# Kernel tuning notes

Hardware: AMD Instinct MI355X
Metric: run time of the kernel (lower is better)

Reference implementation:

```python
import jax, jax.numpy as jnp
import numpy as np

B, T, C = 2, 2048, 2048
N_HEAD = 16
HD = C // N_HEAD  # 128


def setup_inputs() -> dict:
    key = jax.random.key(0)
    k1, k2, k3, k4, k5 = jax.random.split(key, 5)
    s_in = 1.0 / np.sqrt(C)
    return {
        "x": jax.random.normal(k1, (B, T, C), dtype=jnp.float32),
        # weights stored as (in, out), i.e. transpose of torch Linear weight
        "W_attn": jax.random.normal(k2, (C, 3 * C), dtype=jnp.float32) * s_in,
        "b_attn": jax.random.normal(k3, (3 * C,), dtype=jnp.float32) * 0.02,
        "W_proj": jax.random.normal(k4, (C, C), dtype=jnp.float32) * s_in,
        "b_proj": jax.random.normal(k5, (C,), dtype=jnp.float32) * 0.02,
    }


def reference(x, W_attn, b_attn, W_proj, b_proj):
    # qkv projection: (B,T,3C)
    qkv = x @ W_attn + b_attn
    q, k, v = jnp.split(qkv, 3, axis=-1)
    # (B, n_head, T, head_dim)
    q = q.reshape(B, T, N_HEAD, HD).transpose(0, 2, 1, 3)
    k = k.reshape(B, T, N_HEAD, HD).transpose(0, 2, 1, 3)
    v = v.reshape(B, T, N_HEAD, HD).transpose(0, 2, 1, 3)
    # scores (B,H,T,T), causal mask (T_q == T_k prefill path)
    att = jnp.einsum("bhqd,bhkd->bhqk", q, k) * (1.0 / np.sqrt(HD))
    causal = jnp.tril(jnp.ones((T, T), dtype=bool))
    att = jnp.where(causal[None, None], att, -jnp.inf)
    att = jax.nn.softmax(att, axis=-1)  # attn_dropout is identity (p=0)
    y = jnp.einsum("bhqk,bhkd->bhqd", att, v)
    y = y.transpose(0, 2, 1, 3).reshape(B, T, C)
    y = y @ W_proj + b_proj  # resid_dropout identity (p=0)
    # new_cache = (k, v, T) since T == block_size; return output tensor
    return y
```

## Files before the change

kernel.cpp:

```cpp
#include <hip/hip_runtime.h>
#include <cstdint>
#include <cstddef>


typedef __bf16 bf16x8 __attribute__((ext_vector_type(8)));
typedef float  f32x4  __attribute__((ext_vector_type(4)));
typedef unsigned short u16x4 __attribute__((ext_vector_type(4)));
typedef unsigned short u16x8 __attribute__((ext_vector_type(8)));

__device__ __forceinline__ unsigned short f2bf(float f) {
  unsigned int u = __builtin_bit_cast(unsigned int, f);
  u += 0x7fffu + ((u >> 16) & 1u);
  return (unsigned short)(u >> 16);
}

__device__ __forceinline__ void gld16(void* lds, const void* g) {
  __builtin_amdgcn_global_load_lds(
      (const __attribute__((address_space(1))) void*)g,
      (__attribute__((address_space(3))) void*)lds, 16, 0, 0);
}

__device__ __forceinline__ unsigned lds_addr(const void* p) {
  return (unsigned)(size_t)(const __attribute__((address_space(3))) void*)p;
}

__device__ __forceinline__ bf16x8 ds_read16(unsigned addr) {
  bf16x8 r;
  asm volatile("ds_read_b128 %0, %1" : "=v"(r) : "v"(addr));
  return r;
}

__device__ __forceinline__ void ds_write8(unsigned addr, u16x4 d) {
  unsigned long long v = __builtin_bit_cast(unsigned long long, d);
  asm volatile("ds_write_b64 %0, %1" :: "v"(addr), "v"(v));
}

__global__ void cvt_f32_bf16_k(const float* __restrict__ in,
                               unsigned short* __restrict__ out, int n4) {
  int i = blockIdx.x * blockDim.x + threadIdx.x;
  int stride = gridDim.x * blockDim.x;
  for (; i < n4; i += stride) {
    float4 v = ((const float4*)in)[i];
    ushort4 o;
    o.x = f2bf(v.x); o.y = f2bf(v.y); o.z = f2bf(v.z); o.w = f2bf(v.w);
    ((ushort4*)out)[i] = o;
  }
}

__global__ __launch_bounds__(256) void transpose_f32_bf16(
    const float* __restrict__ in, unsigned short* __restrict__ out,
    int R, int C) {
  __shared__ float tile[64][65];
  int c0 = blockIdx.x * 64, r0 = blockIdx.y * 64;
  int t = threadIdx.x;
  int lr = t >> 4, lc = (t & 15) * 4;
#pragma unroll
  for (int i = 0; i < 4; i++) {
    int row = lr + i * 16;
    float4 v = *(const float4*)&in[(size_t)(r0 + row) * C + c0 + lc];
    tile[row][lc] = v.x; tile[row][lc + 1] = v.y;
    tile[row][lc + 2] = v.z; tile[row][lc + 3] = v.w;
  }
  __syncthreads();
  int wr = t >> 3, wc = (t & 7) * 8;
#pragma unroll
  for (int i = 0; i < 2; i++) {
    int crow = wr + i * 32;
    u16x8 o;
#pragma unroll
    for (int j = 0; j < 8; j++) o[j] = f2bf(tile[wc + j][crow]);
    *(u16x8*)&out[(size_t)(c0 + crow) * R + r0 + wc] = o;
  }
}

__global__ __launch_bounds__(256) void extract_vT_k(
    const unsigned short* __restrict__ qkv, unsigned short* __restrict__ vT) {
  __shared__ unsigned int tile32[64][33];
  int bh = blockIdx.z, b = bh >> 4, h = bh & 15;
  int t0 = blockIdx.x * 64, d0 = blockIdx.y * 64;
  int t = threadIdx.x;
  int lr = t >> 3, lc = (t & 7) * 8;
  const unsigned short* src = qkv + (size_t)(b * 2048) * 6144 + 4096 + h * 128;
#pragma unroll
  for (int i = 0; i < 2; i++) {
    int row = lr + i * 32;
    u16x8 v = *(const u16x8*)&src[(size_t)(t0 + row) * 6144 + d0 + lc];
#pragma unroll
    for (int j = 0; j < 8; j++) {
      unsigned short* p = (unsigned short*)&tile32[lc + j][row & 31];
      p[row >> 5] = v[j];
    }
  }
  __syncthreads();
  int dr = t >> 2, tc = (t & 3) * 8;
  u16x8 lo, hi;
#pragma unroll
  for (int j = 0; j < 8; j++) {
    unsigned int u = tile32[dr][tc + j];
    lo[j] = (unsigned short)(u & 0xffffu);
    hi[j] = (unsigned short)(u >> 16);
  }
  unsigned short* dst = vT + (size_t)bh * 128 * 2048 + (size_t)(d0 + dr) * 2048 + t0;
  *(u16x8*)&dst[tc] = lo;
  *(u16x8*)&dst[tc + 32] = hi;
}

template <int OUT_BF16>
__global__ __launch_bounds__(256) void gemm_bt(
    const unsigned short* __restrict__ A, const unsigned short* __restrict__ BT,
    const float* __restrict__ bias, void* __restrict__ Cout,
    int M, int N, int K) {
  __shared__ __align__(16) unsigned short sA[128 * 64];
  __shared__ __align__(16) unsigned short sB[128 * 64];

  const int tid = threadIdx.x, w = tid >> 6, lane = tid & 63;
  const int quad = lane >> 4, l16 = lane & 15;
  const int m0 = blockIdx.y * 128, n0 = blockIdx.x * 128;
  const int wr = w >> 1, wc = w & 1;

  const unsigned short* gA[4];
  const unsigned short* gB[4];
  unsigned short* lA[4];
  unsigned short* lB[4];
#pragma unroll
  for (int i = 0; i < 4; i++) {
    int c = w * 256 + i * 64 + lane;
    int row = c >> 3, scol = (c & 7) ^ (row & 7);
    gA[i] = A + (size_t)(m0 + row) * K + scol * 8;
    gB[i] = BT + (size_t)(n0 + row) * K + scol * 8;
    lA[i] = sA + (size_t)(w * 256 + i * 64) * 8;
    lB[i] = sB + (size_t)(w * 256 + i * 64) * 8;
  }

  f32x4 acc[4][4] = {};

  for (int k0 = 0; k0 < K; k0 += 64) {
#pragma unroll
    for (int i = 0; i < 4; i++) {
      gld16(lA[i], gA[i]); gld16(lB[i], gB[i]);
      gA[i] += 64; gB[i] += 64;
    }
    __syncthreads();

#pragma unroll
    for (int kk = 0; kk < 2; kk++) {
      const int cc = (kk * 4 + quad) ^ (l16 & 7);
      bf16x8 af[4], bfr[4];
#pragma unroll
      for (int mi = 0; mi < 4; mi++)
        af[mi] = *(const bf16x8*)&sA[(wr * 64 + mi * 16 + l16) * 64 + cc * 8];
#pragma unroll
      for (int ni = 0; ni < 4; ni++)
        bfr[ni] = *(const bf16x8*)&sB[(wc * 64 + ni * 16 + l16) * 64 + cc * 8];
#pragma unroll
      for (int mi = 0; mi < 4; mi++)
#pragma unroll
        for (int ni = 0; ni < 4; ni++)
          acc[mi][ni] = __builtin_amdgcn_mfma_f32_16x16x32_bf16(
              af[mi], bfr[ni], acc[mi][ni], 0, 0, 0);
    }
    __syncthreads();
  }

#pragma unroll
  for (int mi = 0; mi < 4; mi++) {
    int row = m0 + wr * 64 + mi * 16 + quad * 4;
#pragma unroll
    for (int ni = 0; ni < 4; ni++) {
      int col = n0 + wc * 64 + ni * 16 + l16;
      float bv = bias[col];
#pragma unroll
      for (int r = 0; r < 4; r++) {
        float v = acc[mi][ni][r] + bv;
        if (OUT_BF16)
          ((unsigned short*)Cout)[(size_t)(row + r) * N + col] = f2bf(v);
        else
          ((float*)Cout)[(size_t)(row + r) * N + col] = v;
      }
    }
  }
}

#define BARRIER8 __builtin_amdgcn_s_barrier()
#define WAIT_LGKM0 asm volatile("s_waitcnt lgkmcnt(0)" ::: "memory")
#define WAIT_LGKM4 asm volatile("s_waitcnt lgkmcnt(4)" ::: "memory")
#define SCHED0 __builtin_amdgcn_sched_barrier(0)
#define WAIT_VM4 asm volatile("s_waitcnt vmcnt(4)" ::: "memory")
#define WAIT_VM0 asm volatile("s_waitcnt vmcnt(0)" ::: "memory")

#define STAGE_A(buf, h, t)                                                   \
  do {                                                                       \
    gld16(&sA[buf][((h) * 1024 + w * 64) * 8],                               \
          gA0 + (size_t)(h) * 128 * K + (size_t)(t) * 64);                   \
    gld16(&sA[buf][((h) * 1024 + 512 + w * 64) * 8],                         \
          gA1 + (size_t)(h) * 128 * K + (size_t)(t) * 64);                   \
  } while (0)

#define STAGE_B(buf, h, t)                                                   \
  do {                                                                       \
    gld16(&sB[buf][((h) * 1024 + w * 64) * 8],                               \
          gB0 + (size_t)(h) * 128 * K + (size_t)(t) * 64);                   \
    gld16(&sB[buf][((h) * 1024 + 512 + w * 64) * 8],                         \
          gB1 + (size_t)(h) * 128 * K + (size_t)(t) * 64);                   \
  } while (0)

#define LDA4(buf, mh, kk)                                                    \
  do {                                                                       \
    const int cc_ = ((kk) * 4 + quad) ^ (l16 & 7);                           \
    _Pragma("unroll") for (int i_ = 0; i_ < 4; ++i_) {                       \
      const int rr_ = (mh) * 128 + wr * 64 + i_ * 16 + l16;                  \
      a_[i_] = ds_read16(lds_addr(&sA[buf][rr_ * 64 + cc_ * 8]));            \
    }                                                                        \
  } while (0)

#define LDB4(buf, kk)                                                        \
  do {                                                                       \
    const int cc_ = ((kk) * 4 + quad) ^ (l16 & 7);                           \
    _Pragma("unroll") for (int i_ = 0; i_ < 4; ++i_) {                       \
      const int rr_ = wc * 64 + i_ * 16 + l16;                               \
      b_[i_] = ds_read16(lds_addr(&sB[buf][rr_ * 64 + cc_ * 8]));            \
    }                                                                        \
  } while (0)

#define MM16(mh)                                                             \
  do {                                                                       \
    __builtin_amdgcn_s_setprio(1);                                           \
    _Pragma("unroll") for (int i_ = 0; i_ < 4; ++i_)                         \
    _Pragma("unroll") for (int n_ = 0; n_ < 4; ++n_)                         \
        acc[(mh) * 4 + i_][n_] = __builtin_amdgcn_mfma_f32_16x16x32_bf16(    \
            a_[i_], b_[n_], acc[(mh) * 4 + i_][n_], 0, 0, 0);                \
    __builtin_amdgcn_s_setprio(0);                                           \
  } while (0)

template <int OUT_BF16>
__global__ __launch_bounds__(512, 2) void gemm_bt8(
    const unsigned short* __restrict__ A, const unsigned short* __restrict__ BT,
    const float* __restrict__ bias, void* __restrict__ Cout,
    int M, int N, int K) {
  __shared__ __align__(16) unsigned short sA[2][256 * 64];
  __shared__ __align__(16) unsigned short sB[2][256 * 64];
  (void)M;

  const int tid = threadIdx.x, w = tid >> 6, lane = tid & 63;
  const int quad = lane >> 4, l16 = lane & 15;
  const int wr = w >> 2, wc = w & 3;

  const int nwgx = gridDim.x;
  const int nwg = nwgx * gridDim.y;
  const int wg = blockIdx.y * nwgx + blockIdx.x;
  const int q8 = nwg >> 3, r8 = nwg & 7;
  const int xcd = wg & 7, loc = wg >> 3;
  const int swz =
      (xcd < r8 ? xcd * (q8 + 1) : r8 * (q8 + 1) + (xcd - r8) * q8) + loc;
  const int m0 = (swz / nwgx) * 256;
  const int n0 = (swz % nwgx) * 256;

  const int c0 = tid, c1 = tid + 512;
  const int r0c = c0 >> 3, s0c = (c0 & 7) ^ (r0c & 7);
  const int r1c = c1 >> 3, s1c = (c1 & 7) ^ (r1c & 7);
  const unsigned short* gA0 = A + (size_t)(m0 + r0c) * K + s0c * 8;
  const unsigned short* gA1 = A + (size_t)(m0 + r1c) * K + s1c * 8;
  const unsigned short* gB0 = BT + (size_t)(n0 + r0c) * K + s0c * 8;
  const unsigned short* gB1 = BT + (size_t)(n0 + r1c) * K + s1c * 8;

  f32x4 acc[8][4] = {};
  bf16x8 a_[4], b_[4];

  const int NT = K >> 6;
  const int NI = NT >> 1;

  STAGE_B(0, 0, 0); STAGE_A(0, 0, 0);
  STAGE_B(0, 1, 0); STAGE_A(0, 1, 0);
  STAGE_B(1, 0, 1); STAGE_A(1, 0, 1);
  WAIT_VM4;
  BARRIER8;

  for (int i = 0; i < NI; ++i) {
    const int t1 = 2 * i + 1;
    const int tn0 = 2 * i + 2, tn1 = 2 * i + 3;
    const bool last = (i == NI - 1);

    LDB4(0, 0); LDA4(0, 0, 0);
    STAGE_B(1, 1, t1); STAGE_A(1, 1, t1);
    BARRIER8; WAIT_LGKM0; SCHED0; MM16(0); BARRIER8;

    LDA4(0, 1, 0);
    BARRIER8; WAIT_LGKM0; SCHED0; MM16(1); BARRIER8;

    LDB4(0, 1); LDA4(0, 0, 1);
    BARRIER8; WAIT_LGKM0; SCHED0; MM16(0); BARRIER8;

    LDA4(0, 1, 1);
    if (!last) {
      STAGE_B(0, 0, tn0); STAGE_A(0, 0, tn0);
      WAIT_VM4;
    } else {
      WAIT_VM0;
    }
    BARRIER8; WAIT_LGKM0; SCHED0; MM16(1); BARRIER8;

    LDB4(1, 0); LDA4(1, 0, 0);
    if (!last) { STAGE_B(0, 1, tn0); STAGE_A(0, 1, tn0); }
    BARRIER8; WAIT_LGKM0; SCHED0; MM16(0); BARRIER8;

    LDA4(1, 1, 0);
    BARRIER8; WAIT_LGKM0; SCHED0; MM16(1); BARRIER8;

    LDB4(1, 1); LDA4(1, 0, 1);
    BARRIER8; WAIT_LGKM0; SCHED0; MM16(0); BARRIER8;

    LDA4(1, 1, 1);
    if (!last) {
      STAGE_B(1, 0, tn1); STAGE_A(1, 0, tn1);
      WAIT_VM4;
    }
    BARRIER8; WAIT_LGKM0; SCHED0; MM16(1); BARRIER8;
  }

#pragma unroll
  for (int mi = 0; mi < 8; ++mi) {
    const int mh = mi >> 2, i2 = mi & 3;
    int row = m0 + mh * 128 + wr * 64 + i2 * 16 + quad * 4;
#pragma unroll
    for (int ni = 0; ni < 4; ++ni) {
      int col = n0 + wc * 64 + ni * 16 + l16;
      float bv = bias[col];
#pragma unroll
      for (int rr = 0; rr < 4; ++rr) {
        float v = acc[mi][ni][rr] + bv;
        if (OUT_BF16)
          ((unsigned short*)Cout)[(size_t)(row + rr) * N + col] = f2bf(v);
        else
          ((float*)Cout)[(size_t)(row + rr) * N + col] = v;
      }
    }
  }
}

#undef STAGE_A
#undef STAGE_B
#undef LDA4
#undef LDB4
#undef MM16

__global__ __launch_bounds__(256) void flash_attn(
    const unsigned short* __restrict__ qkv, const unsigned short* __restrict__ vT,
    unsigned short* __restrict__ yout) {
  __shared__ __align__(16) unsigned short sK[2][64 * 128];
  __shared__ __align__(16) unsigned short sVT[2][128 * 64];
  __shared__ __align__(16) unsigned short sP[4 * 16 * 64];

  const int tid = threadIdx.x, w = tid >> 6, lane = tid & 63;
  const int quad = lane >> 4, l16 = lane & 15;
  const int id = blockIdx.x;
  const int g = id & 31;
  const int qp = id >> 5;
  const int b = g >> 4, h = g & 15;
  const int T = 2048, CC = 6144, HD = 128;
  const float qscale = 0.12753257252f;

  const unsigned short* gK = qkv + (size_t)(b * T) * CC + 2048 + h * HD;
  const unsigned short* gV = vT + (size_t)(b * 16 + h) * HD * T;
  unsigned short* pw = sP + w * 16 * 64;

  const unsigned short* kSrc[4];
  const unsigned short* vSrc[4];
  unsigned short* kDst[4];
  unsigned short* vDst[4];
#pragma unroll
  for (int i = 0; i < 4; i++) {
    int c = w * 256 + i * 64 + lane;
    int kR = c >> 4, kC = (c & 15) ^ (kR & 15);
    int vR = c >> 3, vC = (c & 7) ^ (vR & 7);
    kSrc[i] = gK + (size_t)kR * CC + kC * 8;
    vSrc[i] = gV + (size_t)vR * T + vC * 8;
    kDst[i] = (unsigned short*)sK + (size_t)(w * 256 + i * 64) * 8;
    vDst[i] = (unsigned short*)sVT + (size_t)(w * 256 + i * 64) * 8;
  }
  const int KBUF = 64 * 128, VBUF = 128 * 64;

  const int qtA = qp, qtB = 31 - qp;
  int qt = qtA, kt = 0;

  bf16x8 qf[4];
  float m_old, l_sum;
  f32x4 o[8] = {};
  {
    const size_t qrow = (size_t)(b * T + qt * 64 + w * 16 + l16) * CC + h * HD;
#pragma unroll
    for (int kb = 0; kb < 4; kb++) {
      bf16x8 raw = *(const bf16x8*)&qkv[qrow + kb * 32 + quad * 8];
      bf16x8 sc;
#pragma unroll
      for (int j = 0; j < 8; j++) sc[j] = (__bf16)((float)raw[j] * qscale);
      qf[kb] = sc;
    }
  }
  m_old = -1e30f; l_sum = 0.f;

#pragma unroll
  for (int i = 0; i < 4; i++) {
    gld16(kDst[i], kSrc[i]);
    gld16(vDst[i], vSrc[i]);
  }

  const int total = qtA + qtB + 2;
  for (int it = 0; it < total; ++it) {
    __syncthreads();
    const int cur = it & 1;
    const bool segEnd = (kt == qt);

    if (it + 1 < total) {
      const int nkt = segEnd ? 0 : kt + 1;
      const int nb_ = (it + 1) & 1;
      const size_t kOff = (size_t)nkt * 64 * CC;
      const int vOff = nkt * 64;
#pragma unroll
      for (int i = 0; i < 4; i++) {
        gld16(kDst[i] + (size_t)nb_ * KBUF, kSrc[i] + kOff);
        gld16(vDst[i] + (size_t)nb_ * VBUF, vSrc[i] + vOff);
      }
    }

    const unsigned short* sKc = (const unsigned short*)sK + (size_t)cur * KBUF;
    const unsigned short* sVc = (const unsigned short*)sVT + (size_t)cur * VBUF;

    f32x4 s4[4] = {};
    bf16x8 kf[4], kg[4];
#pragma unroll
    for (int kb = 0; kb < 4; kb++) {
      int rr = kb * 16 + l16;
      int cc = quad ^ l16;
      kf[kb] = ds_read16(lds_addr(&sKc[rr * 128 + cc * 8]));
    }
#pragma unroll
    for (int dc = 0; dc < 4; dc++) {
      if (dc < 3) {
#pragma unroll
        for (int kb = 0; kb < 4; kb++) {
          int rr = kb * 16 + l16;
          int cc = ((dc + 1) * 4 + quad) ^ l16;
          kg[kb] = ds_read16(lds_addr(&sKc[rr * 128 + cc * 8]));
        }
        WAIT_LGKM4;
      } else {
        WAIT_LGKM0;
      }
      SCHED0;
      __builtin_amdgcn_s_setprio(1);
#pragma unroll
      for (int kb = 0; kb < 4; kb++)
        s4[kb] = __builtin_amdgcn_mfma_f32_16x16x32_bf16(kf[kb], qf[dc], s4[kb], 0, 0, 0);
      __builtin_amdgcn_s_setprio(0);
      if (dc < 3) {
#pragma unroll
        for (int kb = 0; kb < 4; kb++) kf[kb] = kg[kb];
      }
    }

    float sv[4][4];
#pragma unroll
    for (int kb = 0; kb < 4; kb++)
#pragma unroll
      for (int r = 0; r < 4; r++) {
        float v = s4[kb][r];
        if (segEnd) {
          if (kb * 16 + quad * 4 + r > w * 16 + l16) v = -1e30f;
        }
        sv[kb][r] = v;
      }

    float mx = sv[0][0];
#pragma unroll
    for (int kb = 0; kb < 4; kb++)
#pragma unroll
      for (int r = 0; r < 4; r++) mx = fmaxf(mx, sv[kb][r]);
    mx = fmaxf(mx, __shfl_xor(mx, 16));
    mx = fmaxf(mx, __shfl_xor(mx, 32));
    float m_new = fmaxf(m_old, mx);
    float a = exp2f(m_old - m_new);
    float ssum = 0.f;
#pragma unroll
    for (int kb = 0; kb < 4; kb++)
#pragma unroll
      for (int r = 0; r < 4; r++) {
        float p = exp2f(sv[kb][r] - m_new);
        sv[kb][r] = p;
        ssum += p;
      }
    ssum += __shfl_xor(ssum, 16);
    ssum += __shfl_xor(ssum, 32);
    l_sum = l_sum * a + ssum;
    m_old = m_new;

    float ar[4];
#pragma unroll
    for (int r = 0; r < 4; r++)
      ar[r] = __shfl(a, (lane & 48) + quad * 4 + r);
#pragma unroll
    for (int nb = 0; nb < 8; nb++)
#pragma unroll
      for (int r = 0; r < 4; r++) o[nb][r] *= ar[r];

#pragma unroll
    for (int kb = 0; kb < 4; kb++) {
      u16x4 pk;
#pragma unroll
      for (int r = 0; r < 4; r++) pk[r] = f2bf(sv[kb][r]);
      int c = kb * 2 + (quad >> 1);
      int cp = c ^ (l16 & 7);
      ds_write8(lds_addr(&pw[l16 * 64 + cp * 8 + (quad & 1) * 4]), pk);
    }
    WAIT_LGKM0;
    SCHED0;

#pragma unroll
    for (int kb2 = 0; kb2 < 2; kb2++) {
      int pcc = (kb2 * 4 + quad) ^ (l16 & 7);
      bf16x8 pf = ds_read16(lds_addr(&pw[l16 * 64 + pcc * 8]));
#pragma unroll
      for (int half = 0; half < 2; half++) {
        bf16x8 vf[4];
#pragma unroll
        for (int j = 0; j < 4; j++) {
          int nb = half * 4 + j;
          int rr = nb * 16 + l16;
          int cc = (kb2 * 4 + quad) ^ (rr & 7);
          vf[j] = ds_read16(lds_addr(&sVc[rr * 64 + cc * 8]));
        }
        WAIT_LGKM0;
        SCHED0;
        __builtin_amdgcn_s_setprio(1);
#pragma unroll
        for (int j = 0; j < 4; j++)
          o[half * 4 + j] = __builtin_amdgcn_mfma_f32_16x16x32_bf16(
              pf, vf[j], o[half * 4 + j], 0, 0, 0);
        __builtin_amdgcn_s_setprio(0);
      }
    }

    if (segEnd) {
      float linv = 1.0f / l_sum;
#pragma unroll
      for (int r = 0; r < 4; r++) {
        float ir = __shfl(linv, (lane & 48) + quad * 4 + r);
        size_t orow = (size_t)(b * T + qt * 64 + w * 16 + quad * 4 + r) * 2048 + h * HD;
#pragma unroll
        for (int nb = 0; nb < 8; nb++)
          yout[orow + nb * 16 + l16] = f2bf(o[nb][r] * ir);
      }
      if (it + 1 < total) {
        qt = qtB;
        const size_t qrow = (size_t)(b * T + qt * 64 + w * 16 + l16) * CC + h * HD;
#pragma unroll
        for (int kb = 0; kb < 4; kb++) {
          bf16x8 raw = *(const bf16x8*)&qkv[qrow + kb * 32 + quad * 8];
          bf16x8 sc;
#pragma unroll
          for (int j = 0; j < 8; j++) sc[j] = (__bf16)((float)raw[j] * qscale);
          qf[kb] = sc;
        }
        m_old = -1e30f; l_sum = 0.f;
#pragma unroll
        for (int nb = 0; nb < 8; nb++) o[nb] = (f32x4){0.f, 0.f, 0.f, 0.f};
      }
      kt = 0;
    } else {
      kt++;
    }
  }
}

extern "C" void kernel_launch(void* const* d_in, const int* in_sizes, int n_in,
                              void* d_out, int out_size, void* d_ws, size_t ws_size,
                              hipStream_t stream) {
  const float* x      = (const float*)d_in[0];
  const float* W_attn = (const float*)d_in[1];
  const float* b_attn = (const float*)d_in[2];
  const float* W_proj = (const float*)d_in[3];
  const float* b_proj = (const float*)d_in[4];
  float* out = (float*)d_out;

  char* ws = (char*)d_ws;
  unsigned short* x_bf  = (unsigned short*)(ws);
  unsigned short* WaT   = (unsigned short*)(ws + 16777216);
  unsigned short* WpT   = (unsigned short*)(ws + 41943040);
  unsigned short* qkv   = (unsigned short*)(ws + 50331648);
  unsigned short* vT    = (unsigned short*)(ws + 100663296);
  unsigned short* y_att = (unsigned short*)(ws + 117440512);

  cvt_f32_bf16_k<<<1024, 256, 0, stream>>>(x, x_bf, 8388608 / 4);
  transpose_f32_bf16<<<dim3(96, 32), 256, 0, stream>>>(W_attn, WaT, 2048, 6144);
  transpose_f32_bf16<<<dim3(32, 32), 256, 0, stream>>>(W_proj, WpT, 2048, 2048);
  gemm_bt8<1><<<dim3(24, 16), 512, 0, stream>>>(x_bf, WaT, b_attn, qkv, 4096, 6144, 2048);
  extract_vT_k<<<dim3(32, 2, 32), 256, 0, stream>>>(qkv, vT);
  flash_attn<<<dim3(512), 256, 0, stream>>>(qkv, vT, y_att);
  gemm_bt<0><<<dim3(16, 32), 256, 0, stream>>>(y_att, WpT, b_proj, out, 4096, 2048, 2048);
}
```

Measured before the change: 379.8 us.

## Pipeline output projection GEMM, add lazy softmax rescale, interleave PV LDS reads

The simple output projection GEMM is replaced by a 512-thread, 256x128-tile kernel. It double-buffers LDS loads, interleaves MFMA with LDS reads under barriers, and maps workgroups to XCDs with a swizzle. In flash attention, the running max is only updated when the block max exceeds it by more than a threshold, which skips the exp and the rescale of the output accumulator in the common case. The PV stage software-pipelines its LDS reads with partial lgkmcnt waits so MFMAs can overlap the reads. The lazy rescale relies on fp32 headroom, allowing probabilities up to 2^8 before the rescale happens.

```diff
diff --git a/kernel.cpp b/kernel.cpp
--- a/kernel.cpp
+++ b/kernel.cpp
@@ -105,85 +105,10 @@
   *(u16x8*)&dst[tc + 32] = hi;
 }
 
-template <int OUT_BF16>
-__global__ __launch_bounds__(256) void gemm_bt(
-    const unsigned short* __restrict__ A, const unsigned short* __restrict__ BT,
-    const float* __restrict__ bias, void* __restrict__ Cout,
-    int M, int N, int K) {
-  __shared__ __align__(16) unsigned short sA[128 * 64];
-  __shared__ __align__(16) unsigned short sB[128 * 64];
-
-  const int tid = threadIdx.x, w = tid >> 6, lane = tid & 63;
-  const int quad = lane >> 4, l16 = lane & 15;
-  const int m0 = blockIdx.y * 128, n0 = blockIdx.x * 128;
-  const int wr = w >> 1, wc = w & 1;
-
-  const unsigned short* gA[4];
-  const unsigned short* gB[4];
-  unsigned short* lA[4];
-  unsigned short* lB[4];
-#pragma unroll
-  for (int i = 0; i < 4; i++) {
-    int c = w * 256 + i * 64 + lane;
-    int row = c >> 3, scol = (c & 7) ^ (row & 7);
-    gA[i] = A + (size_t)(m0 + row) * K + scol * 8;
-    gB[i] = BT + (size_t)(n0 + row) * K + scol * 8;
-    lA[i] = sA + (size_t)(w * 256 + i * 64) * 8;
-    lB[i] = sB + (size_t)(w * 256 + i * 64) * 8;
-  }
-
-  f32x4 acc[4][4] = {};
-
-  for (int k0 = 0; k0 < K; k0 += 64) {
-#pragma unroll
-    for (int i = 0; i < 4; i++) {
-      gld16(lA[i], gA[i]); gld16(lB[i], gB[i]);
-      gA[i] += 64; gB[i] += 64;
-    }
-    __syncthreads();
-
-#pragma unroll
-    for (int kk = 0; kk < 2; kk++) {
-      const int cc = (kk * 4 + quad) ^ (l16 & 7);
-      bf16x8 af[4], bfr[4];
-#pragma unroll
-      for (int mi = 0; mi < 4; mi++)
-        af[mi] = *(const bf16x8*)&sA[(wr * 64 + mi * 16 + l16) * 64 + cc * 8];
-#pragma unroll
-      for (int ni = 0; ni < 4; ni++)
-        bfr[ni] = *(const bf16x8*)&sB[(wc * 64 + ni * 16 + l16) * 64 + cc * 8];
-#pragma unroll
-      for (int mi = 0; mi < 4; mi++)
-#pragma unroll
-        for (int ni = 0; ni < 4; ni++)
-          acc[mi][ni] = __builtin_amdgcn_mfma_f32_16x16x32_bf16(
-              af[mi], bfr[ni], acc[mi][ni], 0, 0, 0);
-    }
-    __syncthreads();
-  }
-
-#pragma unroll
-  for (int mi = 0; mi < 4; mi++) {
-    int row = m0 + wr * 64 + mi * 16 + quad * 4;
-#pragma unroll
-    for (int ni = 0; ni < 4; ni++) {
-      int col = n0 + wc * 64 + ni * 16 + l16;
-      float bv = bias[col];
-#pragma unroll
-      for (int r = 0; r < 4; r++) {
-        float v = acc[mi][ni][r] + bv;
-        if (OUT_BF16)
-          ((unsigned short*)Cout)[(size_t)(row + r) * N + col] = f2bf(v);
-        else
-          ((float*)Cout)[(size_t)(row + r) * N + col] = v;
-      }
-    }
-  }
-}
-
 #define BARRIER8 __builtin_amdgcn_s_barrier()
 #define WAIT_LGKM0 asm volatile("s_waitcnt lgkmcnt(0)" ::: "memory")
 #define WAIT_LGKM4 asm volatile("s_waitcnt lgkmcnt(4)" ::: "memory")
+#define WAIT_LGKM5 asm volatile("s_waitcnt lgkmcnt(5)" ::: "memory")
 #define SCHED0 __builtin_amdgcn_sched_barrier(0)
 #define WAIT_VM4 asm volatile("s_waitcnt vmcnt(4)" ::: "memory")
 #define WAIT_VM0 asm volatile("s_waitcnt vmcnt(0)" ::: "memory")
@@ -343,6 +268,157 @@
 #undef LDB4
 #undef MM16
 
+#define STAGE_Ab(buf, h, t)                                                  \
+  do {                                                                       \
+    gld16(&sA[buf][((h) * 1024 + w * 64) * 8],                               \
+          gA0 + (size_t)(h) * 128 * K + (size_t)(t) * 64);                   \
+    gld16(&sA[buf][((h) * 1024 + 512 + w * 64) * 8],                         \
+          gA1 + (size_t)(h) * 128 * K + (size_t)(t) * 64);                   \
+  } while (0)
+
+#define STAGE_Bb(buf, t)                                                     \
+  do {                                                                       \
+    gld16(&sB[buf][(w * 64) * 8], gB0 + (size_t)(t) * 64);                   \
+    gld16(&sB[buf][(512 + w * 64) * 8], gB1 + (size_t)(t) * 64);             \
+  } while (0)
+
+#define LDA2b(buf, mh2, kk)                                                  \
+  do {                                                                       \
+    const int cc_ = ((kk) * 4 + quad) ^ (l16 & 7);                           \
+    _Pragma("unroll") for (int i_ = 0; i_ < 2; ++i_) {                       \
+      const int rr_ = wr * 64 + ((mh2) * 2 + i_) * 16 + l16;                 \
+      a_[i_] = ds_read16(lds_addr(&sA[buf][rr_ * 64 + cc_ * 8]));            \
+    }                                                                        \
+  } while (0)
+
+#define LDB4b(buf, kk)                                                       \
+  do {                                                                       \
+    const int cc_ = ((kk) * 4 + quad) ^ (l16 & 7);                           \
+    _Pragma("unroll") for (int i_ = 0; i_ < 4; ++i_) {                       \
+      const int rr_ = wc * 64 + i_ * 16 + l16;                               \
+      b_[i_] = ds_read16(lds_addr(&sB[buf][rr_ * 64 + cc_ * 8]));            \
+    }                                                                        \
+  } while (0)
+
+#define MM8b(mh2)                                                            \
+  do {                                                                       \
+    __builtin_amdgcn_s_setprio(1);                                           \
+    _Pragma("unroll") for (int i_ = 0; i_ < 2; ++i_)                         \
+    _Pragma("unroll") for (int n_ = 0; n_ < 4; ++n_)                         \
+        acc[(mh2) * 2 + i_][n_] = __builtin_amdgcn_mfma_f32_16x16x32_bf16(   \
+            a_[i_], b_[n_], acc[(mh2) * 2 + i_][n_], 0, 0, 0);               \
+    __builtin_amdgcn_s_setprio(0);                                           \
+  } while (0)
+
+template <int OUT_BF16>
+__global__ __launch_bounds__(512, 2) void gemm_bt8b(
+    const unsigned short* __restrict__ A, const unsigned short* __restrict__ BT,
+    const float* __restrict__ bias, void* __restrict__ Cout,
+    int M, int N, int K) {
+  __shared__ __align__(16) unsigned short sA[2][256 * 64];
+  __shared__ __align__(16) unsigned short sB[2][128 * 64];
+  (void)M;
+
+  const int tid = threadIdx.x, w = tid >> 6, lane = tid & 63;
+  const int quad = lane >> 4, l16 = lane & 15;
+  const int wr = w >> 1, wc = w & 1;
+
+  const int nwgx = gridDim.x;
+  const int nwg = nwgx * gridDim.y;
+  const int wg = blockIdx.y * nwgx + blockIdx.x;
+  const int q8 = nwg >> 3, r8 = nwg & 7;
+  const int xcd = wg & 7, loc = wg >> 3;
+  const int swz =
+      (xcd < r8 ? xcd * (q8 + 1) : r8 * (q8 + 1) + (xcd - r8) * q8) + loc;
+  const int m0 = (swz / nwgx) * 256;
+  const int n0 = (swz % nwgx) * 128;
+
+  const int c0 = tid, c1 = tid + 512;
+  const int r0c = c0 >> 3, s0c = (c0 & 7) ^ (r0c & 7);
+  const int r1c = c1 >> 3, s1c = (c1 & 7) ^ (r1c & 7);
+  const unsigned short* gA0 = A + (size_t)(m0 + r0c) * K + s0c * 8;
+  const unsigned short* gA1 = A + (size_t)(m0 + r1c) * K + s1c * 8;
+  const unsigned short* gB0 = BT + (size_t)(n0 + r0c) * K + s0c * 8;
+  const unsigned short* gB1 = BT + (size_t)(n0 + r1c) * K + s1c * 8;
+
+  f32x4 acc[4][4] = {};
+  bf16x8 a_[2], b_[4];
+
+  const int NT = K >> 6;
+  const int NI = NT >> 1;
+
+  STAGE_Ab(0, 0, 0); STAGE_Ab(0, 1, 0); STAGE_Bb(0, 0);
+  STAGE_Ab(1, 0, 1); STAGE_Ab(1, 1, 1);
+  WAIT_VM4;
+  BARRIER8;
+
+  for (int i = 0; i < NI; ++i) {
+    const int t1 = 2 * i + 1;
+    const int tn0 = 2 * i + 2, tn1 = 2 * i + 3;
+    const bool last = (i == NI - 1);
+
+    LDB4b(0, 0); LDA2b(0, 0, 0);
+    if (!last) STAGE_Bb(1, t1); else STAGE_Bb(1, t1);
+    BARRIER8; WAIT_LGKM0; SCHED0; MM8b(0); BARRIER8;
+
+    LDA2b(0, 1, 0);
+    BARRIER8; WAIT_LGKM0; SCHED0; MM8b(1); BARRIER8;
+
+    LDB4b(0, 1); LDA2b(0, 0, 1);
+    BARRIER8; WAIT_LGKM0; SCHED0; MM8b(0); BARRIER8;
+
+    LDA2b(0, 1, 1);
+    if (!last) {
+      STAGE_Ab(0, 0, tn0); STAGE_Ab(0, 1, tn0);
+      WAIT_VM4;
+    } else {
+      WAIT_VM0;
+    }
+    BARRIER8; WAIT_LGKM0; SCHED0; MM8b(1); BARRIER8;
+
+    LDB4b(1, 0); LDA2b(1, 0, 0);
+    if (!last) STAGE_Bb(0, tn0);
+    BARRIER8; WAIT_LGKM0; SCHED0; MM8b(0); BARRIER8;
+
+    LDA2b(1, 1, 0);
+    BARRIER8; WAIT_LGKM0; SCHED0; MM8b(1); BARRIER8;
+
+    LDB4b(1, 1); LDA2b(1, 0, 1);
+    BARRIER8; WAIT_LGKM0; SCHED0; MM8b(0); BARRIER8;
+
+    LDA2b(1, 1, 1);
+    if (!last) {
+      STAGE_Ab(1, 0, tn1); STAGE_Ab(1, 1, tn1);
+      WAIT_VM4;
+    }
+    BARRIER8; WAIT_LGKM0; SCHED0; MM8b(1); BARRIER8;
+  }
+
+#pragma unroll
+  for (int mi = 0; mi < 4; ++mi) {
+    int row = m0 + wr * 64 + mi * 16 + quad * 4;
+#pragma unroll
+    for (int ni = 0; ni < 4; ++ni) {
+      int col = n0 + wc * 64 + ni * 16 + l16;
+      float bv = bias[col];
+#pragma unroll
+      for (int rr = 0; rr < 4; ++rr) {
+        float v = acc[mi][ni][rr] + bv;
+        if (OUT_BF16)
+          ((unsigned short*)Cout)[(size_t)(row + rr) * N + col] = f2bf(v);
+        else
+          ((float*)Cout)[(size_t)(row + rr) * N + col] = v;
+      }
+    }
+  }
+}
+
+#undef STAGE_Ab
+#undef STAGE_Bb
+#undef LDA2b
+#undef LDB4b
+#undef MM8b
+
 __global__ __launch_bounds__(256) void flash_attn(
     const unsigned short* __restrict__ qkv, const unsigned short* __restrict__ vT,
     unsigned short* __restrict__ yout) {
@@ -478,7 +554,8 @@
     mx = fmaxf(mx, __shfl_xor(mx, 16));
     mx = fmaxf(mx, __shfl_xor(mx, 32));
     float m_new = fmaxf(m_old, mx);
-    float a = exp2f(m_old - m_new);
+    const bool nogrow = (__all(mx <= m_old + 8.0f) != 0);
+    if (nogrow) m_new = m_old;
     float ssum = 0.f;
 #pragma unroll
     for (int kb = 0; kb < 4; kb++)
@@ -490,17 +567,21 @@
       }
     ssum += __shfl_xor(ssum, 16);
     ssum += __shfl_xor(ssum, 32);
-    l_sum = l_sum * a + ssum;
+    if (nogrow) {
+      l_sum += ssum;
+    } else {
+      float a = exp2f(m_old - m_new);
+      float ar[4];
+#pragma unroll
+      for (int r = 0; r < 4; r++)
+        ar[r] = __shfl(a, (lane & 48) + quad * 4 + r);
+#pragma unroll
+      for (int nb = 0; nb < 8; nb++)
+#pragma unroll
+        for (int r = 0; r < 4; r++) o[nb][r] *= ar[r];
+      l_sum = l_sum * a + ssum;
+    }
     m_old = m_new;
-
-    float ar[4];
-#pragma unroll
-    for (int r = 0; r < 4; r++)
-      ar[r] = __shfl(a, (lane & 48) + quad * 4 + r);
-#pragma unroll
-    for (int nb = 0; nb < 8; nb++)
-#pragma unroll
-      for (int r = 0; r < 4; r++) o[nb][r] *= ar[r];
 
 #pragma unroll
     for (int kb = 0; kb < 4; kb++) {
@@ -514,29 +595,56 @@
     WAIT_LGKM0;
     SCHED0;
 
-#pragma unroll
-    for (int kb2 = 0; kb2 < 2; kb2++) {
-      int pcc = (kb2 * 4 + quad) ^ (l16 & 7);
-      bf16x8 pf = ds_read16(lds_addr(&pw[l16 * 64 + pcc * 8]));
-#pragma unroll
-      for (int half = 0; half < 2; half++) {
-        bf16x8 vf[4];
-#pragma unroll
-        for (int j = 0; j < 4; j++) {
-          int nb = half * 4 + j;
-          int rr = nb * 16 + l16;
-          int cc = (kb2 * 4 + quad) ^ (rr & 7);
-          vf[j] = ds_read16(lds_addr(&sVc[rr * 64 + cc * 8]));
-        }
-        WAIT_LGKM0;
-        SCHED0;
-        __builtin_amdgcn_s_setprio(1);
-#pragma unroll
-        for (int j = 0; j < 4; j++)
-          o[half * 4 + j] = __builtin_amdgcn_mfma_f32_16x16x32_bf16(
-              pf, vf[j], o[half * 4 + j], 0, 0, 0);
-        __builtin_amdgcn_s_setprio(0);
-      }
+    {
+      const int x7 = l16 & 7;
+      const int ccP0 = quad ^ x7, ccP1 = (4 + quad) ^ x7;
+      bf16x8 pf0, pf1, vA[4], vB[4];
+      pf0 = ds_read16(lds_addr(&pw[l16 * 64 + ccP0 * 8]));
+#pragma unroll
+      for (int j = 0; j < 4; j++) {
+        int rr = j * 16 + l16;
+        vA[j] = ds_read16(lds_addr(&sVc[rr * 64 + ccP0 * 8]));
+      }
+#pragma unroll
+      for (int j = 0; j < 4; j++) {
+        int rr = (4 + j) * 16 + l16;
+        vB[j] = ds_read16(lds_addr(&sVc[rr * 64 + ccP0 * 8]));
+      }
+      WAIT_LGKM4; SCHED0;
+      __builtin_amdgcn_s_setprio(1);
+#pragma unroll
+      for (int j = 0; j < 4; j++)
+        o[j] = __builtin_amdgcn_mfma_f32_16x16x32_bf16(pf0, vA[j], o[j], 0, 0, 0);
+      __builtin_amdgcn_s_setprio(0);
+      pf1 = ds_read16(lds_addr(&pw[l16 * 64 + ccP1 * 8]));
+#pragma unroll
+      for (int j = 0; j < 4; j++) {
+        int rr = j * 16 + l16;
+        vA[j] = ds_read16(lds_addr(&sVc[rr * 64 + ccP1 * 8]));
+      }
+      WAIT_LGKM5; SCHED0;
+      __builtin_amdgcn_s_setprio(1);
+#pragma unroll
+      for (int j = 0; j < 4; j++)
+        o[4 + j] = __builtin_amdgcn_mfma_f32_16x16x32_bf16(pf0, vB[j], o[4 + j], 0, 0, 0);
+      __builtin_amdgcn_s_setprio(0);
+#pragma unroll
+      for (int j = 0; j < 4; j++) {
+        int rr = (4 + j) * 16 + l16;
+        vB[j] = ds_read16(lds_addr(&sVc[rr * 64 + ccP1 * 8]));
+      }
+      WAIT_LGKM4; SCHED0;
+      __builtin_amdgcn_s_setprio(1);
+#pragma unroll
+      for (int j = 0; j < 4; j++)
+        o[j] = __builtin_amdgcn_mfma_f32_16x16x32_bf16(pf1, vA[j], o[j], 0, 0, 0);
+      __builtin_amdgcn_s_setprio(0);
+      WAIT_LGKM0; SCHED0;
+      __builtin_amdgcn_s_setprio(1);
+#pragma unroll
+      for (int j = 0; j < 4; j++)
+        o[4 + j] = __builtin_amdgcn_mfma_f32_16x16x32_bf16(pf1, vB[j], o[4 + j], 0, 0, 0);
+      __builtin_amdgcn_s_setprio(0);
     }
 
     if (segEnd) {
@@ -595,5 +703,5 @@
   gemm_bt8<1><<<dim3(24, 16), 512, 0, stream>>>(x_bf, WaT, b_attn, qkv, 4096, 6144, 2048);
   extract_vT_k<<<dim3(32, 2, 32), 256, 0, stream>>>(qkv, vT);
   flash_attn<<<dim3(512), 256, 0, stream>>>(qkv, vT, y_att);
-  gemm_bt<0><<<dim3(16, 32), 256, 0, stream>>>(y_att, WpT, b_proj, out, 4096, 2048, 2048);
-}
+  gemm_bt8b<0><<<dim3(16, 16), 512, 0, stream>>>(y_att, WpT, b_proj, out, 4096, 2048, 2048);
+}
```

Measured after the change: 374.6 us. No clear change (-1.4%).

## Fuse prep kernels, skip lazy softmax rescale, software-pipeline PV LDS reads

Applied to the files above, without the earlier changes.

Merges the x conversion and the two weight transposes into a single prep launch, which removes two kernel launch gaps. In flash attention, the online-softmax rescale of the output accumulator is skipped when no row max grows by more than 8 (log2 units), so the stale max is kept. The PV MFMA loop is restructured to issue the LDS reads for the next fragment group while the current MFMAs run, using partial lgkmcnt waits. The lazy rescale lets exponents reach up to 2^8 before correction, a small numerical risk in exchange for fewer multiplies and shuffles.

```diff
diff --git a/kernel.cpp b/kernel.cpp
--- a/kernel.cpp
+++ b/kernel.cpp
@@ -35,24 +35,9 @@
   asm volatile("ds_write_b64 %0, %1" :: "v"(addr), "v"(v));
 }
 
-__global__ void cvt_f32_bf16_k(const float* __restrict__ in,
-                               unsigned short* __restrict__ out, int n4) {
-  int i = blockIdx.x * blockDim.x + threadIdx.x;
-  int stride = gridDim.x * blockDim.x;
-  for (; i < n4; i += stride) {
-    float4 v = ((const float4*)in)[i];
-    ushort4 o;
-    o.x = f2bf(v.x); o.y = f2bf(v.y); o.z = f2bf(v.z); o.w = f2bf(v.w);
-    ((ushort4*)out)[i] = o;
-  }
-}
-
-__global__ __launch_bounds__(256) void transpose_f32_bf16(
+__device__ __forceinline__ void transpose_tile_64(
     const float* __restrict__ in, unsigned short* __restrict__ out,
-    int R, int C) {
-  __shared__ float tile[64][65];
-  int c0 = blockIdx.x * 64, r0 = blockIdx.y * 64;
-  int t = threadIdx.x;
+    int R, int C, int c0, int r0, int t, float tile[64][65]) {
   int lr = t >> 4, lc = (t & 15) * 4;
 #pragma unroll
   for (int i = 0; i < 4; i++) {
@@ -70,6 +55,30 @@
 #pragma unroll
     for (int j = 0; j < 8; j++) o[j] = f2bf(tile[wc + j][crow]);
     *(u16x8*)&out[(size_t)(c0 + crow) * R + r0 + wc] = o;
+  }
+}
+
+__global__ __launch_bounds__(256) void prep_k(
+    const float* __restrict__ x, const float* __restrict__ W_attn,
+    const float* __restrict__ W_proj, unsigned short* __restrict__ x_bf,
+    unsigned short* __restrict__ WaT, unsigned short* __restrict__ WpT) {
+  __shared__ float tile[64][65];
+  const int bid = blockIdx.x, t = threadIdx.x;
+  if (bid < 3072) {
+    int bx = bid % 96, by = bid / 96;
+    transpose_tile_64(W_attn, WaT, 2048, 6144, bx * 64, by * 64, t, tile);
+  } else if (bid < 4096) {
+    int id = bid - 3072, bx = id & 31, by = id >> 5;
+    transpose_tile_64(W_proj, WpT, 2048, 2048, bx * 64, by * 64, t, tile);
+  } else {
+    const int n4 = 8388608 / 4;
+    int i = (bid - 4096) * 256 + t;
+    for (; i < n4; i += 1024 * 256) {
+      float4 v = ((const float4*)x)[i];
+      ushort4 o;
+      o.x = f2bf(v.x); o.y = f2bf(v.y); o.z = f2bf(v.z); o.w = f2bf(v.w);
+      ((ushort4*)x_bf)[i] = o;
+    }
   }
 }
 
@@ -184,6 +193,7 @@
 #define BARRIER8 __builtin_amdgcn_s_barrier()
 #define WAIT_LGKM0 asm volatile("s_waitcnt lgkmcnt(0)" ::: "memory")
 #define WAIT_LGKM4 asm volatile("s_waitcnt lgkmcnt(4)" ::: "memory")
+#define WAIT_LGKM5 asm volatile("s_waitcnt lgkmcnt(5)" ::: "memory")
 #define SCHED0 __builtin_amdgcn_sched_barrier(0)
 #define WAIT_VM4 asm volatile("s_waitcnt vmcnt(4)" ::: "memory")
 #define WAIT_VM0 asm volatile("s_waitcnt vmcnt(0)" ::: "memory")
@@ -478,7 +488,8 @@
     mx = fmaxf(mx, __shfl_xor(mx, 16));
     mx = fmaxf(mx, __shfl_xor(mx, 32));
     float m_new = fmaxf(m_old, mx);
-    float a = exp2f(m_old - m_new);
+    const bool nogrow = (__all(mx <= m_old + 8.0f) != 0);
+    if (nogrow) m_new = m_old;
     float ssum = 0.f;
 #pragma unroll
     for (int kb = 0; kb < 4; kb++)
@@ -490,17 +501,21 @@
       }
     ssum += __shfl_xor(ssum, 16);
     ssum += __shfl_xor(ssum, 32);
-    l_sum = l_sum * a + ssum;
+    if (nogrow) {
+      l_sum += ssum;
+    } else {
+      float a = exp2f(m_old - m_new);
+      float ar[4];
+#pragma unroll
+      for (int r = 0; r < 4; r++)
+        ar[r] = __shfl(a, (lane & 48) + quad * 4 + r);
+#pragma unroll
+      for (int nb = 0; nb < 8; nb++)
+#pragma unroll
+        for (int r = 0; r < 4; r++) o[nb][r] *= ar[r];
+      l_sum = l_sum * a + ssum;
+    }
     m_old = m_new;
-
-    float ar[4];
-#pragma unroll
-    for (int r = 0; r < 4; r++)
-      ar[r] = __shfl(a, (lane & 48) + quad * 4 + r);
-#pragma unroll
-    for (int nb = 0; nb < 8; nb++)
-#pragma unroll
-      for (int r = 0; r < 4; r++) o[nb][r] *= ar[r];
 
 #pragma unroll
     for (int kb = 0; kb < 4; kb++) {
@@ -514,29 +529,56 @@
     WAIT_LGKM0;
     SCHED0;
 
-#pragma unroll
-    for (int kb2 = 0; kb2 < 2; kb2++) {
-      int pcc = (kb2 * 4 + quad) ^ (l16 & 7);
-      bf16x8 pf = ds_read16(lds_addr(&pw[l16 * 64 + pcc * 8]));
-#pragma unroll
-      for (int half = 0; half < 2; half++) {
-        bf16x8 vf[4];
-#pragma unroll
-        for (int j = 0; j < 4; j++) {
-          int nb = half * 4 + j;
-          int rr = nb * 16 + l16;
-          int cc = (kb2 * 4 + quad) ^ (rr & 7);
-          vf[j] = ds_read16(lds_addr(&sVc[rr * 64 + cc * 8]));
-        }
-        WAIT_LGKM0;
-        SCHED0;
-        __builtin_amdgcn_s_setprio(1);
-#pragma unroll
-        for (int j = 0; j < 4; j++)
-          o[half * 4 + j] = __builtin_amdgcn_mfma_f32_16x16x32_bf16(
-              pf, vf[j], o[half * 4 + j], 0, 0, 0);
-        __builtin_amdgcn_s_setprio(0);
-      }
+    {
+      const int x7 = l16 & 7;
+      const int ccP0 = quad ^ x7, ccP1 = (4 + quad) ^ x7;
+      bf16x8 pf0, pf1, vA[4], vB[4];
+      pf0 = ds_read16(lds_addr(&pw[l16 * 64 + ccP0 * 8]));
+#pragma unroll
+      for (int j = 0; j < 4; j++) {
+        int rr = j * 16 + l16;
+        vA[j] = ds_read16(lds_addr(&sVc[rr * 64 + ccP0 * 8]));
+      }
+#pragma unroll
+      for (int j = 0; j < 4; j++) {
+        int rr = (4 + j) * 16 + l16;
+        vB[j] = ds_read16(lds_addr(&sVc[rr * 64 + ccP0 * 8]));
+      }
+      WAIT_LGKM4; SCHED0;
+      __builtin_amdgcn_s_setprio(1);
+#pragma unroll
+      for (int j = 0; j < 4; j++)
+        o[j] = __builtin_amdgcn_mfma_f32_16x16x32_bf16(pf0, vA[j], o[j], 0, 0, 0);
+      __builtin_amdgcn_s_setprio(0);
+      pf1 = ds_read16(lds_addr(&pw[l16 * 64 + ccP1 * 8]));
+#pragma unroll
+      for (int j = 0; j < 4; j++) {
+        int rr = j * 16 + l16;
+        vA[j] = ds_read16(lds_addr(&sVc[rr * 64 + ccP1 * 8]));
+      }
+      WAIT_LGKM5; SCHED0;
+      __builtin_amdgcn_s_setprio(1);
+#pragma unroll
+      for (int j = 0; j < 4; j++)
+        o[4 + j] = __builtin_amdgcn_mfma_f32_16x16x32_bf16(pf0, vB[j], o[4 + j], 0, 0, 0);
+      __builtin_amdgcn_s_setprio(0);
+#pragma unroll
+      for (int j = 0; j < 4; j++) {
+        int rr = (4 + j) * 16 + l16;
+        vB[j] = ds_read16(lds_addr(&sVc[rr * 64 + ccP1 * 8]));
+      }
+      WAIT_LGKM4; SCHED0;
+      __builtin_amdgcn_s_setprio(1);
+#pragma unroll
+      for (int j = 0; j < 4; j++)
+        o[j] = __builtin_amdgcn_mfma_f32_16x16x32_bf16(pf1, vA[j], o[j], 0, 0, 0);
+      __builtin_amdgcn_s_setprio(0);
+      WAIT_LGKM0; SCHED0;
+      __builtin_amdgcn_s_setprio(1);
+#pragma unroll
+      for (int j = 0; j < 4; j++)
+        o[4 + j] = __builtin_amdgcn_mfma_f32_16x16x32_bf16(pf1, vB[j], o[4 + j], 0, 0, 0);
+      __builtin_amdgcn_s_setprio(0);
     }
 
     if (segEnd) {
@@ -589,9 +631,7 @@
   unsigned short* vT    = (unsigned short*)(ws + 100663296);
   unsigned short* y_att = (unsigned short*)(ws + 117440512);
 
-  cvt_f32_bf16_k<<<1024, 256, 0, stream>>>(x, x_bf, 8388608 / 4);
-  transpose_f32_bf16<<<dim3(96, 32), 256, 0, stream>>>(W_attn, WaT, 2048, 6144);
-  transpose_f32_bf16<<<dim3(32, 32), 256, 0, stream>>>(W_proj, WpT, 2048, 2048);
+  prep_k<<<5120, 256, 0, stream>>>(x, W_attn, W_proj, x_bf, WaT, WpT);
   gemm_bt8<1><<<dim3(24, 16), 512, 0, stream>>>(x_bf, WaT, b_attn, qkv, 4096, 6144, 2048);
   extract_vT_k<<<dim3(32, 2, 32), 256, 0, stream>>>(qkv, vT);
   flash_attn<<<dim3(512), 256, 0, stream>>>(qkv, vT, y_att);
```

Result: faster. 369.9 us (-2.6%).
